# Kernel tuning notes

Measured on AMD Instinct MI355X. Metric: run time of the kernel, lower is better.

Reference implementation:

```python
import jax, jax.numpy as jnp
import numpy as np

N = 100000       # nodes
E = 3200000      # edges
F_IN = 128       # num_node_features
DIM = 32         # hidden dim (fixed in Net1)
L = 3            # num_layers
C = 10           # num_classes


def setup_inputs() -> dict:
    key = jax.random.key(0)
    ks = jax.random.split(key, 16)
    x = jax.random.normal(ks[0], (N, F_IN), dtype=jnp.float32)
    src = jax.random.randint(ks[1], (E,), 0, N, dtype=jnp.int32)
    dst = jax.random.randint(ks[2], (E,), 0, N, dtype=jnp.int32)
    def glorot(k, shape):
        lim = np.sqrt(6.0 / (shape[0] + shape[1])).astype(np.float32)
        return jax.random.uniform(k, shape, jnp.float32, -lim, lim)
    dims = [F_IN, DIM, DIM]
    inp = {"x": x, "src": src, "dst": dst}
    for i in range(L):
        din = dims[i]
        inp[f"Wn{i}"] = glorot(ks[3 + 3 * i], (din, DIM))      # neighbor weight
        inp[f"bn{i}"] = jnp.zeros((DIM,), jnp.float32)          # neighbor bias
        inp[f"Ws{i}"] = glorot(ks[4 + 3 * i], (din, DIM))      # self weight (no bias)
    inp["fc_w"] = glorot(ks[13], (DIM * L + F_IN, C))
    inp["fc_b"] = jnp.zeros((C,), jnp.float32)
    return inp


def _graph_conv_wl(x, src, dst, Wn, bn, Ws):
    # GraphConv(norm='none'): transform then aggregate (sum over in-neighbors)
    h = x @ Wn                                   # [N, DIM]
    msg = h[src]                                 # [E, DIM] gather
    agg = jax.ops.segment_sum(msg, dst, num_segments=N)  # [N, DIM] scatter-add
    return agg + bn + x @ Ws


def reference(x, src, dst, Wn0, bn0, Ws0, Wn1, bn1, Ws1, Wn2, bn2, Ws2, fc_w, fc_b):
    params = [(Wn0, bn0, Ws0), (Wn1, bn1, Ws1), (Wn2, bn2, Ws2)]
    xs = [x]
    h = x
    for Wn, bn, Ws in params:
        h = jax.nn.relu(_graph_conv_wl(h, src, dst, Wn, bn, Ws))
        xs.append(h)
    h = jnp.concatenate(xs, axis=1)              # [N, 128 + 3*32]
    logits = h @ fc_w + fc_b                     # [N, C]
    return jax.nn.log_softmax(logits, axis=1)
```

## Files before the change

### kernel.cpp

```cpp
#include <hip/hip_runtime.h>
#include <cstdint>

#define NN 100000
#define EE 3200000
#define SB_BITS 8
#define SB_NODES (1 << SB_BITS)
#define NSB ((NN + SB_NODES - 1) / SB_NODES)
#define CAP 9216
#define CH 4096
#define EPT (CH / 256)

__device__ inline float4 add4(float4 a, float4 b) {
    return make_float4(a.x + b.x, a.y + b.y, a.z + b.z, a.w + b.w);
}

__device__ inline unsigned pk_bf2(float lo, float hi) {
    unsigned a = __float_as_uint(lo);
    unsigned b = __float_as_uint(hi);
    a = (a + 0x7FFFu + ((a >> 16) & 1u)) >> 16;
    b = (b + 0x7FFFu + ((b >> 16) & 1u)) & 0xFFFF0000u;
    return a | b;
}


__global__ void k_hist_sb(const int* __restrict__ dst, int* __restrict__ scnt) {
    __shared__ int h[NSB];
    for (int i = threadIdx.x; i < NSB; i += 256) h[i] = 0;
    __syncthreads();
    for (int e = blockIdx.x * 256 + threadIdx.x; e < EE; e += gridDim.x * 256)
        atomicAdd(&h[dst[e] >> SB_BITS], 1);
    __syncthreads();
    for (int i = threadIdx.x; i < NSB; i += 256) {
        int v = h[i];
        if (v) atomicAdd(&scnt[i], v);
    }
}

__global__ void k_scan_sb(const int* __restrict__ scnt,
                          int* __restrict__ sbptr, int* __restrict__ cursor) {
    __shared__ int sm[512];
    int i = threadIdx.x;
    int v0 = (i < NSB) ? scnt[i] : 0;
    int v1 = (i + 256 < NSB) ? scnt[i + 256] : 0;
    sm[i] = v0;
    sm[i + 256] = v1;
    __syncthreads();
    for (int o = 1; o < 512; o <<= 1) {
        int a0 = (i >= o) ? sm[i - o] : 0;
        int a1 = (i + 256 >= o) ? sm[i + 256 - o] : 0;
        __syncthreads();
        sm[i] += a0;
        sm[i + 256] += a1;
        __syncthreads();
    }
    if (i < NSB)       { sbptr[i]       = sm[i] - v0;       cursor[i]       = sm[i] - v0; }
    if (i + 256 < NSB) { sbptr[i + 256] = sm[i + 256] - v1; cursor[i + 256] = sm[i + 256] - v1; }
    if (i == 0) sbptr[NSB] = sm[511];
}

__global__ void k_split(const int* __restrict__ src, const int* __restrict__ dst,
                        int* __restrict__ cursor, int* __restrict__ out) {
    __shared__ int hist[512];
    __shared__ int lbase[NSB];
    __shared__ int gbase[NSB];
    __shared__ int buf[CH];
    __shared__ unsigned short keyb[CH];
    const int nchunks = (EE + CH - 1) / CH;
    for (int c = blockIdx.x; c < nchunks; c += gridDim.x) {
        int base = c * CH;
        int cnt = min(CH, EE - base);
        hist[threadIdx.x] = 0;
        hist[threadIdx.x + 256] = 0;
        __syncthreads();
        int words[EPT], ranks[EPT], keys[EPT];
        #pragma unroll
        for (int k = 0; k < EPT; ++k) {
            int idx = threadIdx.x + k * 256;
            if (idx < cnt) {
                int d = dst[base + idx];
                int s = src[base + idx];
                int key = d >> SB_BITS;
                words[k] = s | ((d & (SB_NODES - 1)) << 17);
                keys[k] = key;
                ranks[k] = atomicAdd(&hist[key], 1);
            } else keys[k] = -1;
        }
        __syncthreads();
        int i = threadIdx.x;
        int v0 = hist[i], v1 = hist[i + 256];
        for (int o = 1; o < 512; o <<= 1) {
            int a0 = (i >= o) ? hist[i - o] : 0;
            int a1 = (i + 256 >= o) ? hist[i + 256 - o] : 0;
            __syncthreads();
            hist[i] += a0;
            hist[i + 256] += a1;
            __syncthreads();
        }
        if (i < NSB) {
            lbase[i] = hist[i] - v0;
            gbase[i] = (v0 > 0) ? atomicAdd(&cursor[i], v0) : 0;
        }
        if (i + 256 < NSB) {
            lbase[i + 256] = hist[i + 256] - v1;
            gbase[i + 256] = (v1 > 0) ? atomicAdd(&cursor[i + 256], v1) : 0;
        }
        __syncthreads();
        #pragma unroll
        for (int k = 0; k < EPT; ++k) {
            if (keys[k] >= 0) {
                int p = lbase[keys[k]] + ranks[k];
                buf[p] = words[k];
                keyb[p] = (unsigned short)keys[k];
            }
        }
        __syncthreads();
        for (int j = threadIdx.x; j < cnt; j += 256) {
            int kk = keyb[j];
            out[gbase[kk] + (j - lbase[kk])] = buf[j];
        }
        __syncthreads();
    }
}

__global__ void k_sb_sort(const int* __restrict__ sbptr, const int* __restrict__ packed,
                          int* __restrict__ csr_src, int* __restrict__ rowptr) {
    __shared__ int hist[SB_NODES];
    __shared__ int lbuf[CAP];
    int b = blockIdx.x;
    int e0 = sbptr[b], e1 = sbptr[b + 1];
    int cnt = e1 - e0;
    hist[threadIdx.x] = 0;
    __syncthreads();
    for (int j = e0 + threadIdx.x; j < e1; j += 256)
        atomicAdd(&hist[(packed[j] >> 17) & (SB_NODES - 1)], 1);
    __syncthreads();
    int i = threadIdx.x;
    int v = hist[i];
    for (int o = 1; o < 256; o <<= 1) {
        int a = (i >= o) ? hist[i - o] : 0;
        __syncthreads();
        hist[i] += a;
        __syncthreads();
    }
    int excl = hist[i] - v;
    int node = (b << SB_BITS) + i;
    if (node < NN) rowptr[node] = e0 + excl;
    hist[i] = excl;
    if (b == 0 && i == 0) rowptr[NN] = EE;
    __syncthreads();
    if (cnt <= CAP) {
        for (int j = e0 + threadIdx.x; j < e1; j += 256) {
            int w = packed[j];
            int n = (w >> 17) & (SB_NODES - 1);
            int pos = atomicAdd(&hist[n], 1);
            lbuf[pos] = w & 0x1FFFF;
        }
        __syncthreads();
        for (int j = threadIdx.x; j < cnt; j += 256)
            csr_src[e0 + j] = lbuf[j];
    } else {
        for (int j = e0 + threadIdx.x; j < e1; j += 256) {
            int w = packed[j];
            int n = (w >> 17) & (SB_NODES - 1);
            int pos = atomicAdd(&hist[n], 1);
            csr_src[e0 + pos] = w & 0x1FFFF;
        }
    }
}


template <int DIN>
__global__ __launch_bounds__(64, 2) void k_transform(
        const float* __restrict__ h,
        const float* __restrict__ Wn,
        const float* __restrict__ Ws,
        const float* __restrict__ bn,
        unsigned* __restrict__ t_bf,
        float* __restrict__ hout) {
    const int half = blockIdx.x & 1;
    const int d0 = half * 16;
    const int node = (blockIdx.x >> 1) * 64 + threadIdx.x;
    if (node >= NN) return;
    const float* __restrict__ hr = h + (size_t)node * DIN;
    float accn[16], accs[16];
    #pragma unroll
    for (int d = 0; d < 16; ++d) { accn[d] = 0.f; accs[d] = 0.f; }
    constexpr int NK4 = DIN / 4;
    float4 f0 = *(const float4*)(hr);
    float4 f1 = *(const float4*)(hr + 4);
    float4 f2 = *(const float4*)(hr + 8);
    #pragma unroll 2
    for (int k4 = 0; k4 < NK4; ++k4) {
        float4 cur = f0;
        f0 = f1;
        f1 = f2;
        if (k4 + 3 < NK4) f2 = *(const float4*)(hr + (k4 + 3) * 4);
        float fj[4] = {cur.x, cur.y, cur.z, cur.w};
        #pragma unroll
        for (int j = 0; j < 4; ++j) {
            float fv = fj[j];
            const float* __restrict__ wn = Wn + (k4 * 4 + j) * 32 + d0;
            const float* __restrict__ ws = Ws + (k4 * 4 + j) * 32 + d0;
            #pragma unroll
            for (int d = 0; d < 16; ++d) {
                accn[d] = fmaf(fv, wn[d], accn[d]);
                accs[d] = fmaf(fv, ws[d], accs[d]);
            }
        }
    }
    unsigned tb[8];
    #pragma unroll
    for (int d = 0; d < 8; ++d) tb[d] = pk_bf2(accn[2 * d], accn[2 * d + 1]);
    unsigned* tp = t_bf + (size_t)node * 16 + half * 8;
    *(uint4*)(tp + 0) = make_uint4(tb[0], tb[1], tb[2], tb[3]);
    *(uint4*)(tp + 4) = make_uint4(tb[4], tb[5], tb[6], tb[7]);
    float* __restrict__ hp = hout + (size_t)node * 32 + d0;
    #pragma unroll
    for (int d = 0; d < 16; d += 4)
        *(float4*)(hp + d) = make_float4(accs[d] + bn[d0 + d], accs[d + 1] + bn[d0 + d + 1],
                                         accs[d + 2] + bn[d0 + d + 2], accs[d + 3] + bn[d0 + d + 3]);
}

__global__ void k_aggregate(const int* __restrict__ rowptr,
                            const int* __restrict__ csr_src,
                            const uint2* __restrict__ t2,
                            float4* __restrict__ hout4) {
    int node = blockIdx.x * 32 + (threadIdx.x >> 3);
    int q = threadIdx.x & 7;
    if (node >= NN) return;
    int j = rowptr[node];
    int end = rowptr[node + 1];
    float4 a0 = make_float4(0.f, 0.f, 0.f, 0.f);
    float4 a1 = a0, a2 = a0, a3 = a0;
    for (; j + 4 <= end; j += 4) {
        int s0 = csr_src[j];
        int s1 = csr_src[j + 1];
        int s2 = csr_src[j + 2];
        int s3 = csr_src[j + 3];
        uint2 u0 = t2[s0 * 8 + q];
        uint2 u1 = t2[s1 * 8 + q];
        uint2 u2 = t2[s2 * 8 + q];
        uint2 u3 = t2[s3 * 8 + q];
        a0.x += __uint_as_float(u0.x << 16); a0.y += __uint_as_float(u0.x & 0xFFFF0000u);
        a0.z += __uint_as_float(u0.y << 16); a0.w += __uint_as_float(u0.y & 0xFFFF0000u);
        a1.x += __uint_as_float(u1.x << 16); a1.y += __uint_as_float(u1.x & 0xFFFF0000u);
        a1.z += __uint_as_float(u1.y << 16); a1.w += __uint_as_float(u1.y & 0xFFFF0000u);
        a2.x += __uint_as_float(u2.x << 16); a2.y += __uint_as_float(u2.x & 0xFFFF0000u);
        a2.z += __uint_as_float(u2.y << 16); a2.w += __uint_as_float(u2.y & 0xFFFF0000u);
        a3.x += __uint_as_float(u3.x << 16); a3.y += __uint_as_float(u3.x & 0xFFFF0000u);
        a3.z += __uint_as_float(u3.y << 16); a3.w += __uint_as_float(u3.y & 0xFFFF0000u);
    }
    for (; j < end; ++j) {
        uint2 u = t2[csr_src[j] * 8 + q];
        a0.x += __uint_as_float(u.x << 16); a0.y += __uint_as_float(u.x & 0xFFFF0000u);
        a0.z += __uint_as_float(u.y << 16); a0.w += __uint_as_float(u.y & 0xFFFF0000u);
    }
    float4 s = add4(add4(a0, a1), add4(a2, a3));
    int idx = node * 8 + q;
    float4 h = hout4[idx];
    h.x = fmaxf(h.x + s.x, 0.f);
    h.y = fmaxf(h.y + s.y, 0.f);
    h.z = fmaxf(h.z + s.z, 0.f);
    h.w = fmaxf(h.w + s.w, 0.f);
    hout4[idx] = h;
}

__global__ void k_final(const float* __restrict__ x,
                        const float* __restrict__ h1,
                        const float* __restrict__ h2,
                        const float* __restrict__ h3,
                        const float* __restrict__ fc_w,
                        const float* __restrict__ fc_b,
                        float* __restrict__ out) {
    __shared__ float Wl[224 * 10];
    __shared__ float bl[10];
    for (int i = threadIdx.x; i < 224 * 10; i += blockDim.x) Wl[i] = fc_w[i];
    if (threadIdx.x < 10) bl[threadIdx.x] = fc_b[threadIdx.x];
    __syncthreads();
    int n = blockIdx.x * blockDim.x + threadIdx.x;
    if (n >= NN) return;
    float acc[10];
    #pragma unroll
    for (int c = 0; c < 10; ++c) acc[c] = bl[c];
    const float4* xr4 = (const float4*)(x + (size_t)n * 128);
    for (int j4 = 0; j4 < 32; ++j4) {
        float4 f = xr4[j4];
        #pragma unroll
        for (int c = 0; c < 10; ++c) acc[c] += f.x * Wl[(j4 * 4 + 0) * 10 + c];
        #pragma unroll
        for (int c = 0; c < 10; ++c) acc[c] += f.y * Wl[(j4 * 4 + 1) * 10 + c];
        #pragma unroll
        for (int c = 0; c < 10; ++c) acc[c] += f.z * Wl[(j4 * 4 + 2) * 10 + c];
        #pragma unroll
        for (int c = 0; c < 10; ++c) acc[c] += f.w * Wl[(j4 * 4 + 3) * 10 + c];
    }
    const float* hs[3] = {h1, h2, h3};
    for (int l = 0; l < 3; ++l) {
        const float4* hr4 = (const float4*)(hs[l] + (size_t)n * 32);
        const int base = 128 + l * 32;
        for (int j4 = 0; j4 < 8; ++j4) {
            float4 f = hr4[j4];
            #pragma unroll
            for (int c = 0; c < 10; ++c) acc[c] += f.x * Wl[(base + j4 * 4 + 0) * 10 + c];
            #pragma unroll
            for (int c = 0; c < 10; ++c) acc[c] += f.y * Wl[(base + j4 * 4 + 1) * 10 + c];
            #pragma unroll
            for (int c = 0; c < 10; ++c) acc[c] += f.z * Wl[(base + j4 * 4 + 2) * 10 + c];
            #pragma unroll
            for (int c = 0; c < 10; ++c) acc[c] += f.w * Wl[(base + j4 * 4 + 3) * 10 + c];
        }
    }
    float m = acc[0];
    #pragma unroll
    for (int c = 1; c < 10; ++c) m = fmaxf(m, acc[c]);
    float s = 0.f;
    #pragma unroll
    for (int c = 0; c < 10; ++c) s += __expf(acc[c] - m);
    float ls = __logf(s);
    #pragma unroll
    for (int c = 0; c < 10; ++c) out[n * 10 + c] = acc[c] - m - ls;
}

extern "C" void kernel_launch(void* const* d_in, const int* in_sizes, int n_in,
                              void* d_out, int out_size, void* d_ws, size_t ws_size,
                              hipStream_t stream) {
    const float* x   = (const float*)d_in[0];
    const int*   src = (const int*)d_in[1];
    const int*   dst = (const int*)d_in[2];
    const float* Wn[3] = {(const float*)d_in[3], (const float*)d_in[6], (const float*)d_in[9]};
    const float* bn[3] = {(const float*)d_in[4], (const float*)d_in[7], (const float*)d_in[10]};
    const float* Ws[3] = {(const float*)d_in[5], (const float*)d_in[8], (const float*)d_in[11]};
    const float* fc_w = (const float*)d_in[12];
    const float* fc_b = (const float*)d_in[13];
    float* out = (float*)d_out;

    char* w = (char*)d_ws;
    const size_t NF = (size_t)NN * 32;
    unsigned* t_bf = (unsigned*)w;              w += (size_t)NN * 16 * 4;
    float* h1  = (float*)w;                     w += NF * 4;
    float* h2  = (float*)w;                     w += NF * 4;
    float* h3  = (float*)w;                     w += NF * 4;
    int* csr_src = (int*)w;                     w += (size_t)EE * 4;
    int* scnt   = (int*)w;                      w += (size_t)NSB * 4;
    int* sbptr  = (int*)w;                      w += (size_t)(NSB + 1) * 4;
    int* cursor = (int*)w;                      w += (size_t)NSB * 4;
    int* rowptr = (int*)w;                      w += (size_t)(NN + 1) * 4;
    int* packed = (int*)h3;

    hipMemsetAsync(scnt, 0, (size_t)NSB * 4, stream);
    k_hist_sb<<<512, 256, 0, stream>>>(dst, scnt);
    k_scan_sb<<<1, 256, 0, stream>>>(scnt, sbptr, cursor);
    k_split<<<512, 256, 0, stream>>>(src, dst, cursor, packed);
    k_sb_sort<<<NSB, 256, 0, stream>>>(sbptr, packed, csr_src, rowptr);

    const int tr_blocks = 2 * ((NN + 63) / 64);
    const int ag_blocks = (NN + 31) / 32;
    k_transform<128><<<tr_blocks, 64, 0, stream>>>(x, Wn[0], Ws[0], bn[0], t_bf, h1);
    k_aggregate<<<ag_blocks, 256, 0, stream>>>(rowptr, csr_src, (const uint2*)t_bf, (float4*)h1);
    k_transform<32><<<tr_blocks, 64, 0, stream>>>(h1, Wn[1], Ws[1], bn[1], t_bf, h2);
    k_aggregate<<<ag_blocks, 256, 0, stream>>>(rowptr, csr_src, (const uint2*)t_bf, (float4*)h2);
    k_transform<32><<<tr_blocks, 64, 0, stream>>>(h2, Wn[2], Ws[2], bn[2], t_bf, h3);
    k_aggregate<<<ag_blocks, 256, 0, stream>>>(rowptr, csr_src, (const uint2*)t_bf, (float4*)h3);
    k_final<<<(NN + 255) / 256, 256, 0, stream>>>(x, h1, h2, h3, fc_w, fc_b, out);
}
```

Before: 429.3 us.

## Retile transform kernel: 256-thread blocks, two nodes per lane, 8 output dims per wave

```diff
diff --git a/kernel.cpp b/kernel.cpp
--- a/kernel.cpp
+++ b/kernel.cpp
@@ -170,55 +170,83 @@
 
 
 template <int DIN>
-__global__ __launch_bounds__(64, 2) void k_transform(
+__global__ __launch_bounds__(256, 4) void k_transform(
         const float* __restrict__ h,
         const float* __restrict__ Wn,
         const float* __restrict__ Ws,
         const float* __restrict__ bn,
         unsigned* __restrict__ t_bf,
         float* __restrict__ hout) {
-    const int half = blockIdx.x & 1;
-    const int d0 = half * 16;
-    const int node = (blockIdx.x >> 1) * 64 + threadIdx.x;
-    if (node >= NN) return;
-    const float* __restrict__ hr = h + (size_t)node * DIN;
-    float accn[16], accs[16];
-    #pragma unroll
-    for (int d = 0; d < 16; ++d) { accn[d] = 0.f; accs[d] = 0.f; }
+    const int wq = __builtin_amdgcn_readfirstlane(threadIdx.x >> 6);
+    const int d0 = wq * 8;
+    const int lane = threadIdx.x & 63;
+    const int n0 = blockIdx.x * 128 + lane;
+    const int n1 = n0 + 64;
+    const bool v0 = n0 < NN;
+    const bool v1 = n1 < NN;
+    const float* __restrict__ hr0 = h + (size_t)(v0 ? n0 : NN - 1) * DIN;
+    const float* __restrict__ hr1 = h + (size_t)(v1 ? n1 : NN - 1) * DIN;
+    float an0[8], as0[8], an1[8], as1[8];
+    #pragma unroll
+    for (int d = 0; d < 8; ++d) { an0[d] = 0.f; as0[d] = 0.f; an1[d] = 0.f; as1[d] = 0.f; }
     constexpr int NK4 = DIN / 4;
-    float4 f0 = *(const float4*)(hr);
-    float4 f1 = *(const float4*)(hr + 4);
-    float4 f2 = *(const float4*)(hr + 8);
+    float4 a0 = *(const float4*)(hr0);
+    float4 a1 = *(const float4*)(hr0 + 4);
+    float4 a2 = *(const float4*)(hr0 + 8);
+    float4 b0 = *(const float4*)(hr1);
+    float4 b1 = *(const float4*)(hr1 + 4);
+    float4 b2 = *(const float4*)(hr1 + 8);
     #pragma unroll 2
     for (int k4 = 0; k4 < NK4; ++k4) {
-        float4 cur = f0;
-        f0 = f1;
-        f1 = f2;
-        if (k4 + 3 < NK4) f2 = *(const float4*)(hr + (k4 + 3) * 4);
-        float fj[4] = {cur.x, cur.y, cur.z, cur.w};
+        float4 ca = a0; a0 = a1; a1 = a2;
+        float4 cb = b0; b0 = b1; b1 = b2;
+        if (k4 + 3 < NK4) {
+            a2 = *(const float4*)(hr0 + (k4 + 3) * 4);
+            b2 = *(const float4*)(hr1 + (k4 + 3) * 4);
+        }
+        float fja[4] = {ca.x, ca.y, ca.z, ca.w};
+        float fjb[4] = {cb.x, cb.y, cb.z, cb.w};
         #pragma unroll
         for (int j = 0; j < 4; ++j) {
-            float fv = fj[j];
+            float fa = fja[j];
+            float fb = fjb[j];
             const float* __restrict__ wn = Wn + (k4 * 4 + j) * 32 + d0;
             const float* __restrict__ ws = Ws + (k4 * 4 + j) * 32 + d0;
             #pragma unroll
-            for (int d = 0; d < 16; ++d) {
-                accn[d] = fmaf(fv, wn[d], accn[d]);
-                accs[d] = fmaf(fv, ws[d], accs[d]);
+            for (int d = 0; d < 8; ++d) {
+                float wv = wn[d];
+                float sv = ws[d];
+                an0[d] = fmaf(fa, wv, an0[d]);
+                an1[d] = fmaf(fb, wv, an1[d]);
+                as0[d] = fmaf(fa, sv, as0[d]);
+                as1[d] = fmaf(fb, sv, as1[d]);
             }
         }
     }
-    unsigned tb[8];
-    #pragma unroll
-    for (int d = 0; d < 8; ++d) tb[d] = pk_bf2(accn[2 * d], accn[2 * d + 1]);
-    unsigned* tp = t_bf + (size_t)node * 16 + half * 8;
-    *(uint4*)(tp + 0) = make_uint4(tb[0], tb[1], tb[2], tb[3]);
-    *(uint4*)(tp + 4) = make_uint4(tb[4], tb[5], tb[6], tb[7]);
-    float* __restrict__ hp = hout + (size_t)node * 32 + d0;
-    #pragma unroll
-    for (int d = 0; d < 16; d += 4)
-        *(float4*)(hp + d) = make_float4(accs[d] + bn[d0 + d], accs[d + 1] + bn[d0 + d + 1],
-                                         accs[d + 2] + bn[d0 + d + 2], accs[d + 3] + bn[d0 + d + 3]);
+    if (v0) {
+        unsigned t0 = pk_bf2(an0[0], an0[1]);
+        unsigned t1 = pk_bf2(an0[2], an0[3]);
+        unsigned t2 = pk_bf2(an0[4], an0[5]);
+        unsigned t3 = pk_bf2(an0[6], an0[7]);
+        *(uint4*)(t_bf + (size_t)n0 * 16 + wq * 4) = make_uint4(t0, t1, t2, t3);
+        float* hp = hout + (size_t)n0 * 32 + d0;
+        *(float4*)(hp + 0) = make_float4(as0[0] + bn[d0 + 0], as0[1] + bn[d0 + 1],
+                                         as0[2] + bn[d0 + 2], as0[3] + bn[d0 + 3]);
+        *(float4*)(hp + 4) = make_float4(as0[4] + bn[d0 + 4], as0[5] + bn[d0 + 5],
+                                         as0[6] + bn[d0 + 6], as0[7] + bn[d0 + 7]);
+    }
+    if (v1) {
+        unsigned t0 = pk_bf2(an1[0], an1[1]);
+        unsigned t1 = pk_bf2(an1[2], an1[3]);
+        unsigned t2 = pk_bf2(an1[4], an1[5]);
+        unsigned t3 = pk_bf2(an1[6], an1[7]);
+        *(uint4*)(t_bf + (size_t)n1 * 16 + wq * 4) = make_uint4(t0, t1, t2, t3);
+        float* hp = hout + (size_t)n1 * 32 + d0;
+        *(float4*)(hp + 0) = make_float4(as1[0] + bn[d0 + 0], as1[1] + bn[d0 + 1],
+                                         as1[2] + bn[d0 + 2], as1[3] + bn[d0 + 3]);
+        *(float4*)(hp + 4) = make_float4(as1[4] + bn[d0 + 4], as1[5] + bn[d0 + 5],
+                                         as1[6] + bn[d0 + 6], as1[7] + bn[d0 + 7]);
+    }
 }
 
 __global__ void k_aggregate(const int* __restrict__ rowptr,
@@ -353,13 +381,13 @@
     k_split<<<512, 256, 0, stream>>>(src, dst, cursor, packed);
     k_sb_sort<<<NSB, 256, 0, stream>>>(sbptr, packed, csr_src, rowptr);
 
-    const int tr_blocks = 2 * ((NN + 63) / 64);
+    const int tr_blocks = (NN + 127) / 128;
     const int ag_blocks = (NN + 31) / 32;
-    k_transform<128><<<tr_blocks, 64, 0, stream>>>(x, Wn[0], Ws[0], bn[0], t_bf, h1);
+    k_transform<128><<<tr_blocks, 256, 0, stream>>>(x, Wn[0], Ws[0], bn[0], t_bf, h1);
     k_aggregate<<<ag_blocks, 256, 0, stream>>>(rowptr, csr_src, (const uint2*)t_bf, (float4*)h1);
-    k_transform<32><<<tr_blocks, 64, 0, stream>>>(h1, Wn[1], Ws[1], bn[1], t_bf, h2);
+    k_transform<32><<<tr_blocks, 256, 0, stream>>>(h1, Wn[1], Ws[1], bn[1], t_bf, h2);
     k_aggregate<<<ag_blocks, 256, 0, stream>>>(rowptr, csr_src, (const uint2*)t_bf, (float4*)h2);
-    k_transform<32><<<tr_blocks, 64, 0, stream>>>(h2, Wn[2], Ws[2], bn[2], t_bf, h3);
+    k_transform<32><<<tr_blocks, 256, 0, stream>>>(h2, Wn[2], Ws[2], bn[2], t_bf, h3);
     k_aggregate<<<ag_blocks, 256, 0, stream>>>(rowptr, csr_src, (const uint2*)t_bf, (float4*)h3);
     k_final<<<(NN + 255) / 256, 256, 0, stream>>>(x, h1, h2, h3, fc_w, fc_b, out);
 }
```

New measurement: 425.1 us. About the same (-1.0%).
